# Performance work log

Hardware: AMD Instinct MI355X
Metric: run time of the kernel (lower is better)

## Reference

```python
import jax, jax.numpy as jnp
import numpy as np
from jax import lax

B, H, W, C = 4, 96, 96, 256
F = 256
KH = KW = 3
K = KH * KW
DG = 1
CG = C // DG
SH = SW = 1
DH = DW = 1
PAD_T = (DH * (KH - 1)) // 2  # 'same' padding (top/left) for 3x3 dil 1
PAD_L = (DW * (KW - 1)) // 2


def setup_inputs() -> dict:
    key = jax.random.key(0)
    k1, k2, k3 = jax.random.split(key, 3)
    x = jax.random.normal(k1, (B, H, W, C), jnp.float32)
    # offset/mask conv weights (orig init zeros; small random to exercise sampling)
    om_kernel = jax.random.normal(k2, (KH, KW, C, DG * 3 * K), jnp.float32) * 0.01
    om_bias = jnp.zeros((DG * 3 * K,), jnp.float32)
    stdv = 1.0 / np.sqrt(C * KH * KW)
    kernel = jax.random.uniform(k3, (K * C, F), jnp.float32, -stdv, stdv)
    bias = jnp.zeros((F,), jnp.float32)
    return {"x": x, "om_kernel": om_kernel, "om_bias": om_bias, "kernel": kernel, "bias": bias}


def reference(x, om_kernel, om_bias, kernel, bias):
    Bx, Hx, Wx, Cx = x.shape
    # offset/mask prediction conv (NHWC, 'SAME', matches keras Conv2D)
    om = lax.conv_general_dilated(
        x, om_kernel, (SH, SW), "SAME", rhs_dilation=(DH, DW),
        dimension_numbers=("NHWC", "HWIO", "NHWC")) + om_bias
    Ho, Wo = om.shape[1], om.shape[2]
    off = om[..., : 2 * DG * K].reshape(Bx, Ho, Wo, DG, K, 2)  # (dy, dx) per group/kpoint
    mask = jax.nn.sigmoid(om[..., 2 * DG * K :]).reshape(Bx, Ho, Wo, DG, K) * 2.0

    # base sampling grid: y = ho*SH - PAD_T + ki*DH (+ dy), similarly x
    base_y = (jnp.arange(Ho) * SH - PAD_T)[:, None] + (jnp.arange(KH) * DH)[None, :]  # [Ho,KH]
    base_x = (jnp.arange(Wo) * SW - PAD_L)[:, None] + (jnp.arange(KW) * DW)[None, :]  # [Wo,KW]
    gy = jnp.broadcast_to(base_y[:, None, :, None], (Ho, Wo, KH, KW)).reshape(Ho, Wo, K)
    gx = jnp.broadcast_to(base_x[None, :, None, :], (Ho, Wo, KH, KW)).reshape(Ho, Wo, K)

    py = gy[None, :, :, None, :].astype(x.dtype) + off[..., 0]  # [B,Ho,Wo,DG,K]
    px = gx[None, :, :, None, :].astype(x.dtype) + off[..., 1]

    # reorder to [B, N, DG] with N = Ho*Wo*K (K varies fastest after spatial)
    N = Ho * Wo * K
    py = py.transpose(0, 1, 2, 4, 3).reshape(Bx, N, DG)
    px = px.transpose(0, 1, 2, 4, 3).reshape(Bx, N, DG)
    mask_t = mask.transpose(0, 1, 2, 4, 3).reshape(Bx, N, DG)

    y0 = jnp.floor(py)
    x0 = jnp.floor(px)
    fy = py - y0
    fx = px - x0

    xf = x.reshape(Bx, Hx * Wx, DG, CG)
    val = jnp.zeros((Bx, N, DG, CG), x.dtype)
    for yi, wy in ((y0, 1.0 - fy), (y0 + 1.0, fy)):
        for xi, wx in ((x0, 1.0 - fx), (x0 + 1.0, fx)):
            valid = (yi >= 0) & (yi < Hx) & (xi >= 0) & (xi < Wx)
            yc = jnp.clip(yi, 0, Hx - 1).astype(jnp.int32)
            xc = jnp.clip(xi, 0, Wx - 1).astype(jnp.int32)
            lin = yc * Wx + xc  # [B,N,DG]
            g = jnp.take_along_axis(xf, lin[..., None], axis=1)  # [B,N,DG,CG]
            val = val + g * (wy * wx * valid.astype(x.dtype))[..., None]

    # modulate and im2col -> GEMM
    cols = (val * mask_t[..., None]).reshape(Bx, Ho * Wo, K * Cx)
    out = jnp.matmul(cols, kernel).reshape(Bx, Ho, Wo, -1) + bias
    return out
```

## Files before the change

### kernel.cpp

```cpp
#include <hip/hip_runtime.h>
#include <hip/hip_bf16.h>
#include <stdint.h>
#include <stddef.h>


namespace {
constexpr int H  = 96, W = 96, C = 256, F = 256;
constexpr int HP = 98;
constexpr int NP = 4 * 96 * 96;
constexpr int KC = 9 * 256;

constexpr int NB_PAD  = 4 * HP * HP / 8;
constexpr int NB_OMW  = 9 * 32;
constexpr int NB_WT   = (KC / 64) * (F / 64);
}

typedef __attribute__((ext_vector_type(8))) short bf16x8;
typedef __attribute__((ext_vector_type(4))) float floatx4;

__device__ __forceinline__ void load_lds16(const void* g, void* l) {
  __builtin_amdgcn_global_load_lds((const __attribute__((address_space(1))) void*)g,
                                   (__attribute__((address_space(3))) void*)l,
                                   16, 0, 0);
}

__device__ __forceinline__ uint32_t pk2(float lo, float hi) {
  __hip_bfloat162 t = __float22bfloat162_rn(float2{lo, hi});
  return *reinterpret_cast<uint32_t*>(&t);
}

__device__ __forceinline__ void acc8(uint4 v, float w, float* a) {
  a[0] += w * __uint_as_float(v.x << 16); a[1] += w * __uint_as_float(v.x & 0xffff0000u);
  a[2] += w * __uint_as_float(v.y << 16); a[3] += w * __uint_as_float(v.y & 0xffff0000u);
  a[4] += w * __uint_as_float(v.z << 16); a[5] += w * __uint_as_float(v.z & 0xffff0000u);
  a[6] += w * __uint_as_float(v.w << 16); a[7] += w * __uint_as_float(v.w & 0xffff0000u);
}

__global__ __launch_bounds__(256) void k_pad(const float* __restrict__ x,
                                             uint4* __restrict__ xp4) {
  const int tid = threadIdx.x;
  const int sub = tid >> 5, cid = tid & 31;
  const int pp  = blockIdx.x * 8 + sub;
  const int b   = pp / (HP * HP);
  const int r   = pp % (HP * HP);
  const int y   = r / HP, xq = r % HP;
  uint4 o = {0u, 0u, 0u, 0u};
  if (y >= 1 && y <= H && xq >= 1 && xq <= W) {
    const float* src = x + ((size_t)((b * H + (y - 1)) * W + (xq - 1))) * C + cid * 8;
    const float4 v0 = *(const float4*)src;
    const float4 v1 = *(const float4*)(src + 4);
    o.x = pk2(v0.x, v0.y); o.y = pk2(v0.z, v0.w);
    o.z = pk2(v1.x, v1.y); o.w = pk2(v1.z, v1.w);
  }
  xp4[(size_t)pp * 32 + cid] = o;
}

__global__ __launch_bounds__(256) void k_wprep(const float* __restrict__ omk,
                                               const float* __restrict__ kern,
                                               __hip_bfloat16* __restrict__ wom,
                                               __hip_bfloat16* __restrict__ wt) {
  __shared__ float t[64][65];
  const int bi = blockIdx.x, tid = threadIdx.x;

  if (bi < NB_OMW) {
    const int kk = bi / 32, oc = bi % 32;
    float v = (oc < 27) ? omk[(size_t)(kk * 256 + tid) * 27 + oc] : 0.f;
    wom[(size_t)oc * KC + kk * 256 + tid] = __float2bfloat16(v);
  } else {
    const int j   = bi - NB_OMW;
    const int kc0 = (j % (KC / 64)) * 64, f0 = (j / (KC / 64)) * 64;
    const int rr = tid >> 6, cc = tid & 63;
#pragma unroll
    for (int i = 0; i < 16; ++i)
      t[rr * 16 + i][cc] = kern[(size_t)(kc0 + rr * 16 + i) * F + f0 + cc];
    __syncthreads();
#pragma unroll
    for (int i = 0; i < 16; ++i) {
      const int frow = rr * 16 + i;
      wt[(size_t)(f0 + frow) * KC + kc0 + cc] = __float2bfloat16(t[cc][frow]);
    }
  }
}

__global__ __launch_bounds__(256) void k_omgemm(const __hip_bfloat16* __restrict__ xp,
                                                const __hip_bfloat16* __restrict__ wom,
                                                float* __restrict__ pOm) {
  __shared__ __align__(16) char lds[49152];
  const int tid  = threadIdx.x;
  const int xr   = blockIdx.x;
  const int xs   = (xr & 7) * 72 + (xr >> 3);
  const int m0   = xs * 64;
  const int lane = tid & 63, wave = tid >> 6;
  const int quad = lane >> 4, l16 = lane & 15;

  const int srow = tid >> 4;
  const int gchk = (tid & 15) ^ srow;

  const __hip_bfloat16* abase[4];
#pragma unroll
  for (int j = 0; j < 4; ++j) {
    const int p  = m0 + srow + j * 16;
    const int b  = p / (H * W);
    const int hw = p % (H * W);
    const int h  = hw / W, w = hw % W;
    abase[j] = xp + ((size_t)(b * HP + h) * HP + w) * C + gchk * 8;
  }
  const __hip_bfloat16* bbase[2];
#pragma unroll
  for (int j = 0; j < 2; ++j)
    bbase[j] = wom + (size_t)(srow + j * 16) * KC + gchk * 8;

  auto stage = [&](int buf, int k0) {
    const int kk = k0 >> 8, c0 = k0 & 255;
    const int aoff = ((kk / 3) * HP + (kk % 3)) * C + c0;
    char* base = &lds[buf * 24576];
#pragma unroll
    for (int j = 0; j < 4; ++j)
      load_lds16(abase[j] + aoff, base + j * 4096 + tid * 16);
#pragma unroll
    for (int j = 0; j < 2; ++j)
      load_lds16(bbase[j] + k0, base + 16384 + j * 4096 + tid * 16);
  };

  floatx4 acc[2];
  acc[0] = (floatx4){0.f, 0.f, 0.f, 0.f};
  acc[1] = (floatx4){0.f, 0.f, 0.f, 0.f};

  stage(0, 0);
  int cur = 0;
#pragma unroll 1
  for (int k0 = 0; k0 < KC; k0 += 128) {
    __syncthreads();
    if (k0 + 128 < KC) stage(cur ^ 1, k0 + 128);
    const char* base = &lds[cur * 24576];

#pragma unroll
    for (int ks = 0; ks < 4; ++ks) {
      const int slot = (((ks * 4 + quad) ^ l16) & 15) * 16;
      bf16x8 af = *(const bf16x8*)&base[(wave * 16 + l16) * 256 + slot];
      bf16x8 b0 = *(const bf16x8*)&base[16384 + l16 * 256 + slot];
      bf16x8 b1 = *(const bf16x8*)&base[16384 + (16 + l16) * 256 + slot];
      acc[0] = __builtin_amdgcn_mfma_f32_16x16x32_bf16(af, b0, acc[0], 0, 0, 0);
      acc[1] = __builtin_amdgcn_mfma_f32_16x16x32_bf16(af, b1, acc[1], 0, 0, 0);
    }
    cur ^= 1;
  }

#pragma unroll
  for (int nt = 0; nt < 2; ++nt) {
    const int gm = m0 + wave * 16 + quad * 4;
    const int gn = nt * 16 + l16;
#pragma unroll
    for (int r = 0; r < 4; ++r)
      pOm[(size_t)(gm + r) * 32 + gn] = acc[nt][r];
  }
}

__global__ __launch_bounds__(256) void k_sample(const uint4* __restrict__ xp4,
                                                const float* __restrict__ pOm,
                                                const float* __restrict__ om_bias,
                                                uint4* __restrict__ cols4) {
  __shared__ float2 s_ow[8][9][4];

  const int tid = threadIdx.x;
  const int sub = tid >> 5, cid = tid & 31;
  const int bs  = (blockIdx.x & 7) * 576 + (blockIdx.x >> 3);

  if (tid < 72) {
    const int ps = tid / 9, k = tid % 9;
    const int p  = bs * 8 + ps;
    const int b  = p / (H * W);
    const int hw = p % (H * W);
    const int h = hw / W, w = hw % W;
    const float dy = om_bias[2 * k]     + pOm[(size_t)p * 32 + 2 * k];
    const float dx = om_bias[2 * k + 1] + pOm[(size_t)p * 32 + 2 * k + 1];
    const float mv = om_bias[18 + k]    + pOm[(size_t)p * 32 + 18 + k];
    const float m  = 2.f / (1.f + __expf(-mv));
    const float sy = (float)(h - 1 + k / 3) + dy;
    const float sx = (float)(w - 1 + k % 3) + dx;
    const float y0f = floorf(sy), x0f = floorf(sx);
    const float fy = sy - y0f, fx = sx - x0f;
    const int y0 = (int)y0f, x0 = (int)x0f;
#pragma unroll
    for (int c2 = 0; c2 < 4; ++c2) {
      const int dy2 = c2 >> 1, dx2 = c2 & 1;
      const int yi = y0 + dy2, xi = x0 + dx2;
      const bool valid = (yi >= 0) & (yi < H) & (xi >= 0) & (xi < W);
      const float wgt = valid ? (dy2 ? fy : 1.f - fy) * (dx2 ? fx : 1.f - fx) * m : 0.f;
      const int yc = min(max(yi + 1, 0), HP - 1);
      const int xc = min(max(xi + 1, 0), HP - 1);
      const int off = ((b * HP + yc) * HP + xc) * 32;
      s_ow[ps][k][c2] = float2{__int_as_float(off), wgt};
    }
  }
  __syncthreads();

  const int p = bs * 8 + sub;
  uint4* __restrict__ ob = cols4 + (size_t)p * 288 + cid;

#pragma unroll 1
  for (int k = 0; k < 9; ++k) {
    const float2 ow0 = s_ow[sub][k][0], ow1 = s_ow[sub][k][1];
    const float2 ow2 = s_ow[sub][k][2], ow3 = s_ow[sub][k][3];
    float a[8] = {0.f, 0.f, 0.f, 0.f, 0.f, 0.f, 0.f, 0.f};
    acc8(xp4[(size_t)__float_as_int(ow0.x) + cid], ow0.y, a);
    acc8(xp4[(size_t)__float_as_int(ow1.x) + cid], ow1.y, a);
    acc8(xp4[(size_t)__float_as_int(ow2.x) + cid], ow2.y, a);
    acc8(xp4[(size_t)__float_as_int(ow3.x) + cid], ow3.y, a);
    uint4 o;
    o.x = pk2(a[0], a[1]); o.y = pk2(a[2], a[3]);
    o.z = pk2(a[4], a[5]); o.w = pk2(a[6], a[7]);
    ob[k * 32] = o;
  }
}

__global__ __launch_bounds__(256) void k_gemm(const __hip_bfloat16* __restrict__ A,
                                              const __hip_bfloat16* __restrict__ Bt,
                                              const float* __restrict__ bias,
                                              float* __restrict__ out) {
  __shared__ __align__(16) char lds[28672];

  const int tid  = threadIdx.x;
  const int u    = (blockIdx.x & 7) * 96 + (blockIdx.x >> 3);
  const int m0   = (u >> 1) * 96;
  const int n0   = (u & 1) * 128;
  const int lane = tid & 63, wave = tid >> 6;
  const int wm = wave & 1, wn = wave >> 1;
  const int quad = lane >> 4, l16 = lane & 15;

  const int row = tid >> 2, kp = (tid & 3) ^ ((tid >> 3) & 3);
  const __hip_bfloat16* a0 = A  + (size_t)(m0 + row) * KC + kp * 8;
  const __hip_bfloat16* a1 = A  + (size_t)(m0 + 64 + row) * KC + kp * 8;
  const __hip_bfloat16* b0 = Bt + (size_t)(n0 + row) * KC + kp * 8;
  const __hip_bfloat16* b1 = Bt + (size_t)(n0 + 64 + row) * KC + kp * 8;

  auto stage = [&](int buf, int k0) {
    char* base = &lds[buf * 14336];
    load_lds16(a0 + k0, base + tid * 16);
    if (tid < 128) load_lds16(a1 + k0, base + 4096 + tid * 16);
    load_lds16(b0 + k0, base + 6144 + tid * 16);
    load_lds16(b1 + k0, base + 10240 + tid * 16);
  };

  floatx4 acc[3][4];
#pragma unroll
  for (int i = 0; i < 3; ++i)
#pragma unroll
    for (int j = 0; j < 4; ++j) acc[i][j] = (floatx4){0.f, 0.f, 0.f, 0.f};

  const int swq = (quad ^ ((l16 >> 1) & 3)) * 16;

  stage(0, 0);
  int cur = 0;
#pragma unroll 1
  for (int k0 = 0; k0 < KC; k0 += 32) {
    __syncthreads();
    if (k0 + 32 < KC) stage(cur ^ 1, k0 + 32);
    const char* base = &lds[cur * 14336];

    bf16x8 af[3], bfr[4];
#pragma unroll
    for (int mt = 0; mt < 3; ++mt)
      af[mt] = *(const bf16x8*)&base[(wm * 48 + mt * 16 + l16) * 64 + swq];
#pragma unroll
    for (int nt = 0; nt < 4; ++nt)
      bfr[nt] = *(const bf16x8*)&base[6144 + (wn * 64 + nt * 16 + l16) * 64 + swq];
#pragma unroll
    for (int mt = 0; mt < 3; ++mt)
#pragma unroll
      for (int nt = 0; nt < 4; ++nt)
        acc[mt][nt] = __builtin_amdgcn_mfma_f32_16x16x32_bf16(af[mt], bfr[nt], acc[mt][nt], 0, 0, 0);
    cur ^= 1;
  }

#pragma unroll
  for (int mt = 0; mt < 3; ++mt) {
#pragma unroll
    for (int nt = 0; nt < 4; ++nt) {
      const int gm = m0 + wm * 48 + mt * 16 + quad * 4;
      const int gn = n0 + wn * 64 + nt * 16 + l16;
      const float bs = bias[gn];
#pragma unroll
      for (int r = 0; r < 4; ++r)
        out[(size_t)(gm + r) * F + gn] = acc[mt][nt][r] + bs;
    }
  }
}

extern "C" void kernel_launch(void* const* d_in, const int* in_sizes, int n_in,
                              void* d_out, int out_size, void* d_ws, size_t ws_size,
                              hipStream_t stream) {
  const float* x    = (const float*)d_in[0];
  const float* omk  = (const float*)d_in[1];
  const float* omb  = (const float*)d_in[2];
  const float* kern = (const float*)d_in[3];
  const float* bias = (const float*)d_in[4];
  float* out = (float*)d_out;

  char* ws = (char*)d_ws;
  size_t off = 0;
  __hip_bfloat16* wt   = (__hip_bfloat16*)(ws + off); off += (size_t)F * KC * 2;
  __hip_bfloat16* xp   = (__hip_bfloat16*)(ws + off); off += (size_t)4 * HP * HP * C * 2;
  __hip_bfloat16* wom  = (__hip_bfloat16*)(ws + off); off += (size_t)32 * KC * 2;
  float*          pOm  = (float*)(ws + off);          off += (size_t)NP * 32 * 4;
  __hip_bfloat16* cols = (__hip_bfloat16*)(ws + off);

  k_pad   <<<dim3(NB_PAD),         256, 0, stream>>>(x, (uint4*)xp);
  k_wprep <<<dim3(NB_OMW + NB_WT), 256, 0, stream>>>(omk, kern, wom, wt);
  k_omgemm<<<dim3(576),            256, 0, stream>>>(xp, wom, pOm);
  k_sample<<<dim3(NP / 8),         256, 0, stream>>>((const uint4*)xp, pOm, omb, (uint4*)cols);
  k_gemm  <<<dim3(768),            256, 0, stream>>>(cols, wt, bias, out);
}
```

Measured before the change: 201.4 us.

## Reorder deformable conv as per-tap GEMM then bilinear combine

Replaces the sample-then-GEMM pipeline with nine per-tap GEMMs over the dense input (x·W_k for every pixel), stored as bf16 in G, followed by a combine kernel that bilinearly gathers the projected 256-wide features and sums over taps with mask weights. This relies on bilinear interpolation being linear, so projection can happen before sampling, and it removes the large im2col cols buffer. It also fuses bias into the combine kernel. In exchange it writes and reads a 9×NP×256 bf16 intermediate, and rounding the per-tap outputs to bf16 before summing adds precision error.

```diff
diff --git a/kernel.cpp b/kernel.cpp
--- a/kernel.cpp
+++ b/kernel.cpp
@@ -156,10 +156,85 @@
   }
 }
 
-__global__ __launch_bounds__(256) void k_sample(const uint4* __restrict__ xp4,
-                                                const float* __restrict__ pOm,
-                                                const float* __restrict__ om_bias,
-                                                uint4* __restrict__ cols4) {
+__global__ __launch_bounds__(512) void k_gemmG(const __hip_bfloat16* __restrict__ xp,
+                                               const __hip_bfloat16* __restrict__ wt,
+                                               __hip_bfloat16* __restrict__ G) {
+  __shared__ __align__(16) char lds[49152];
+  const int tid   = threadIdx.x;
+  const int xs    = (blockIdx.x & 7) * 36 + (blockIdx.x >> 3);
+  const int m0    = xs * 128;
+  const int kk    = blockIdx.y;
+  const int kbase = kk * 256;
+  const int lane  = tid & 63, wave = tid >> 6;
+  const int wm = wave >> 2, wn = wave & 3;
+  const int quad = lane >> 4, l16 = lane & 15;
+
+  const int kp = (tid & 3) ^ ((tid >> 3) & 3);
+  const int p  = m0 + (tid >> 2);
+  const int b  = p / (H * W);
+  const int hw = p % (H * W);
+  const int h  = hw / W, w = hw % W;
+  const __hip_bfloat16* asrc = xp + ((size_t)((b * HP + h + 1) * HP) + w + 1) * C + kp * 8;
+  const __hip_bfloat16* b0   = wt + (size_t)(tid >> 2) * KC + kbase + kp * 8;
+  const __hip_bfloat16* b1   = b0 + (size_t)128 * KC;
+
+  auto stage = [&](int buf, int c0) {
+    char* base = &lds[buf * 24576];
+    load_lds16(asrc + c0, base + tid * 16);
+    load_lds16(b0 + c0, base + 8192 + tid * 16);
+    load_lds16(b1 + c0, base + 16384 + tid * 16);
+  };
+
+  floatx4 acc[4][4];
+#pragma unroll
+  for (int i = 0; i < 4; ++i)
+#pragma unroll
+    for (int j = 0; j < 4; ++j) acc[i][j] = (floatx4){0.f, 0.f, 0.f, 0.f};
+
+  const int swq = (quad ^ ((l16 >> 1) & 3)) * 16;
+
+  stage(0, 0);
+  int cur = 0;
+#pragma unroll 1
+  for (int c0 = 0; c0 < 256; c0 += 32) {
+    __syncthreads();
+    if (c0 + 32 < 256) stage(cur ^ 1, c0 + 32);
+    const char* base = &lds[cur * 24576];
+
+    bf16x8 af[4], bfr[4];
+#pragma unroll
+    for (int mt = 0; mt < 4; ++mt)
+      af[mt] = *(const bf16x8*)&base[(wm * 64 + mt * 16 + l16) * 64 + swq];
+#pragma unroll
+    for (int nt = 0; nt < 4; ++nt)
+      bfr[nt] = *(const bf16x8*)&base[8192 + (wn * 64 + nt * 16 + l16) * 64 + swq];
+#pragma unroll
+    for (int mt = 0; mt < 4; ++mt)
+#pragma unroll
+      for (int nt = 0; nt < 4; ++nt)
+        acc[mt][nt] = __builtin_amdgcn_mfma_f32_16x16x32_bf16(af[mt], bfr[nt], acc[mt][nt], 0, 0, 0);
+    cur ^= 1;
+  }
+
+  __hip_bfloat16* gp = G + (size_t)kk * NP * 256;
+#pragma unroll
+  for (int mt = 0; mt < 4; ++mt) {
+#pragma unroll
+    for (int nt = 0; nt < 4; ++nt) {
+      const int gm = m0 + wm * 64 + mt * 16 + quad * 4;
+      const int gn = wn * 64 + nt * 16 + l16;
+#pragma unroll
+      for (int r = 0; r < 4; ++r)
+        gp[(size_t)(gm + r) * 256 + gn] = __float2bfloat16(acc[mt][nt][r]);
+    }
+  }
+}
+
+__global__ __launch_bounds__(256) void k_combine(const uint4* __restrict__ G4,
+                                                 const float* __restrict__ pOm,
+                                                 const float* __restrict__ om_bias,
+                                                 const float* __restrict__ bias,
+                                                 float* __restrict__ out) {
   __shared__ float2 s_ow[8][9][4];
 
   const int tid = threadIdx.x;
@@ -187,104 +262,34 @@
       const int yi = y0 + dy2, xi = x0 + dx2;
       const bool valid = (yi >= 0) & (yi < H) & (xi >= 0) & (xi < W);
       const float wgt = valid ? (dy2 ? fy : 1.f - fy) * (dx2 ? fx : 1.f - fx) * m : 0.f;
-      const int yc = min(max(yi + 1, 0), HP - 1);
-      const int xc = min(max(xi + 1, 0), HP - 1);
-      const int off = ((b * HP + yc) * HP + xc) * 32;
+      const int yc = min(max(yi, 0), H - 1);
+      const int xc = min(max(xi, 0), W - 1);
+      const int off = ((b * H + yc) * W + xc) * 32;
       s_ow[ps][k][c2] = float2{__int_as_float(off), wgt};
     }
   }
   __syncthreads();
 
   const int p = bs * 8 + sub;
-  uint4* __restrict__ ob = cols4 + (size_t)p * 288 + cid;
+  float a[8] = {0.f, 0.f, 0.f, 0.f, 0.f, 0.f, 0.f, 0.f};
 
 #pragma unroll 1
   for (int k = 0; k < 9; ++k) {
     const float2 ow0 = s_ow[sub][k][0], ow1 = s_ow[sub][k][1];
     const float2 ow2 = s_ow[sub][k][2], ow3 = s_ow[sub][k][3];
-    float a[8] = {0.f, 0.f, 0.f, 0.f, 0.f, 0.f, 0.f, 0.f};
-    acc8(xp4[(size_t)__float_as_int(ow0.x) + cid], ow0.y, a);
-    acc8(xp4[(size_t)__float_as_int(ow1.x) + cid], ow1.y, a);
-    acc8(xp4[(size_t)__float_as_int(ow2.x) + cid], ow2.y, a);
-    acc8(xp4[(size_t)__float_as_int(ow3.x) + cid], ow3.y, a);
-    uint4 o;
-    o.x = pk2(a[0], a[1]); o.y = pk2(a[2], a[3]);
-    o.z = pk2(a[4], a[5]); o.w = pk2(a[6], a[7]);
-    ob[k * 32] = o;
-  }
-}
-
-__global__ __launch_bounds__(256) void k_gemm(const __hip_bfloat16* __restrict__ A,
-                                              const __hip_bfloat16* __restrict__ Bt,
-                                              const float* __restrict__ bias,
-                                              float* __restrict__ out) {
-  __shared__ __align__(16) char lds[28672];
-
-  const int tid  = threadIdx.x;
-  const int u    = (blockIdx.x & 7) * 96 + (blockIdx.x >> 3);
-  const int m0   = (u >> 1) * 96;
-  const int n0   = (u & 1) * 128;
-  const int lane = tid & 63, wave = tid >> 6;
-  const int wm = wave & 1, wn = wave >> 1;
-  const int quad = lane >> 4, l16 = lane & 15;
-
-  const int row = tid >> 2, kp = (tid & 3) ^ ((tid >> 3) & 3);
-  const __hip_bfloat16* a0 = A  + (size_t)(m0 + row) * KC + kp * 8;
-  const __hip_bfloat16* a1 = A  + (size_t)(m0 + 64 + row) * KC + kp * 8;
-  const __hip_bfloat16* b0 = Bt + (size_t)(n0 + row) * KC + kp * 8;
-  const __hip_bfloat16* b1 = Bt + (size_t)(n0 + 64 + row) * KC + kp * 8;
-
-  auto stage = [&](int buf, int k0) {
-    char* base = &lds[buf * 14336];
-    load_lds16(a0 + k0, base + tid * 16);
-    if (tid < 128) load_lds16(a1 + k0, base + 4096 + tid * 16);
-    load_lds16(b0 + k0, base + 6144 + tid * 16);
-    load_lds16(b1 + k0, base + 10240 + tid * 16);
-  };
-
-  floatx4 acc[3][4];
-#pragma unroll
-  for (int i = 0; i < 3; ++i)
-#pragma unroll
-    for (int j = 0; j < 4; ++j) acc[i][j] = (floatx4){0.f, 0.f, 0.f, 0.f};
-
-  const int swq = (quad ^ ((l16 >> 1) & 3)) * 16;
-
-  stage(0, 0);
-  int cur = 0;
-#pragma unroll 1
-  for (int k0 = 0; k0 < KC; k0 += 32) {
-    __syncthreads();
-    if (k0 + 32 < KC) stage(cur ^ 1, k0 + 32);
-    const char* base = &lds[cur * 14336];
-
-    bf16x8 af[3], bfr[4];
-#pragma unroll
-    for (int mt = 0; mt < 3; ++mt)
-      af[mt] = *(const bf16x8*)&base[(wm * 48 + mt * 16 + l16) * 64 + swq];
-#pragma unroll
-    for (int nt = 0; nt < 4; ++nt)
-      bfr[nt] = *(const bf16x8*)&base[6144 + (wn * 64 + nt * 16 + l16) * 64 + swq];
-#pragma unroll
-    for (int mt = 0; mt < 3; ++mt)
-#pragma unroll
-      for (int nt = 0; nt < 4; ++nt)
-        acc[mt][nt] = __builtin_amdgcn_mfma_f32_16x16x32_bf16(af[mt], bfr[nt], acc[mt][nt], 0, 0, 0);
-    cur ^= 1;
-  }
-
-#pragma unroll
-  for (int mt = 0; mt < 3; ++mt) {
-#pragma unroll
-    for (int nt = 0; nt < 4; ++nt) {
-      const int gm = m0 + wm * 48 + mt * 16 + quad * 4;
-      const int gn = n0 + wn * 64 + nt * 16 + l16;
-      const float bs = bias[gn];
-#pragma unroll
-      for (int r = 0; r < 4; ++r)
-        out[(size_t)(gm + r) * F + gn] = acc[mt][nt][r] + bs;
-    }
-  }
+    const uint4* pk = G4 + (size_t)k * (NP * 32) + cid;
+    acc8(pk[(size_t)__float_as_int(ow0.x)], ow0.y, a);
+    acc8(pk[(size_t)__float_as_int(ow1.x)], ow1.y, a);
+    acc8(pk[(size_t)__float_as_int(ow2.x)], ow2.y, a);
+    acc8(pk[(size_t)__float_as_int(ow3.x)], ow3.y, a);
+  }
+
+  const float* bp = bias + cid * 8;
+  float* op = out + (size_t)p * 256 + cid * 8;
+  float4 o0 = {a[0] + bp[0], a[1] + bp[1], a[2] + bp[2], a[3] + bp[3]};
+  float4 o1 = {a[4] + bp[4], a[5] + bp[5], a[6] + bp[6], a[7] + bp[7]};
+  *(float4*)op = o0;
+  *(float4*)(op + 4) = o1;
 }
 
 extern "C" void kernel_launch(void* const* d_in, const int* in_sizes, int n_in,
@@ -303,11 +308,11 @@
   __hip_bfloat16* xp   = (__hip_bfloat16*)(ws + off); off += (size_t)4 * HP * HP * C * 2;
   __hip_bfloat16* wom  = (__hip_bfloat16*)(ws + off); off += (size_t)32 * KC * 2;
   float*          pOm  = (float*)(ws + off);          off += (size_t)NP * 32 * 4;
-  __hip_bfloat16* cols = (__hip_bfloat16*)(ws + off);
-
-  k_pad   <<<dim3(NB_PAD),         256, 0, stream>>>(x, (uint4*)xp);
-  k_wprep <<<dim3(NB_OMW + NB_WT), 256, 0, stream>>>(omk, kern, wom, wt);
-  k_omgemm<<<dim3(576),            256, 0, stream>>>(xp, wom, pOm);
-  k_sample<<<dim3(NP / 8),         256, 0, stream>>>((const uint4*)xp, pOm, omb, (uint4*)cols);
-  k_gemm  <<<dim3(768),            256, 0, stream>>>(cols, wt, bias, out);
-}
+  __hip_bfloat16* G    = (__hip_bfloat16*)(ws + off);
+
+  k_pad    <<<dim3(NB_PAD),          256, 0, stream>>>(x, (uint4*)xp);
+  k_wprep  <<<dim3(NB_OMW + NB_WT),  256, 0, stream>>>(omk, kern, wom, wt);
+  k_omgemm <<<dim3(576),             256, 0, stream>>>(xp, wom, pOm);
+  k_gemmG  <<<dim3(288, 9),          512, 0, stream>>>(xp, wt, G);
+  k_combine<<<dim3(NP / 8),          256, 0, stream>>>((const uint4*)G, pOm, omb, bias, out);
+}
```

After: 217.4 us. 1.08x slower.
